# Performance work log

Hardware: AMD Instinct MI355X
Metric: run time of the kernel (lower is better)

## Reference

```python
import jax, jax.numpy as jnp
import numpy as np
from jax import lax

EPS = 1e-6
PPU = 256        # points_per_unit
MULT = 8         # 2 ** rho.num_halving_layers
C = 3            # in_channels (data channels)
NBASIS = 5
NS = 4           # num_samples
RHO_IN = 16      # encoder out / rho in channels
RHO_OUT = 32     # rho out channels
KW = 5           # conv kernel width


def setup_inputs() -> dict:
    key = jax.random.key(0)
    ks = jax.random.split(key, 16)
    nb, npts, ntar = 16, 2048, 256
    x = jax.random.uniform(ks[0], (nb, npts, C), jnp.float32)
    y = jax.random.normal(ks[1], (nb, npts, C), jnp.float32)
    x_out = jax.random.uniform(ks[2], (nb, ntar, C), jnp.float32)
    # --- compute_xgrid (done concretely at setup; mirrors torch logic) ---
    x_min = float(min(np.min(np.asarray(x)), np.min(np.asarray(x_out)))) - 0.1
    x_max = float(max(np.max(np.asarray(x)), np.max(np.asarray(x_out)))) + 0.1
    ngrid = int(np.ceil(PPU * (x_max - x_min) / MULT) * MULT)  # to_multiple
    grid = jnp.linspace(x_min, x_max, ngrid, dtype=jnp.float32)
    x_grid = jnp.broadcast_to(grid[None, :, None], (nb, ngrid, C))
    # --- parameters ---
    init_l = 2.0 / PPU
    enc_sigma = jnp.log(1e-6 + init_l * jnp.ones((C,), jnp.float32))
    int_sigma = jnp.log(1e-6 + init_l * jnp.ones((NBASIS, C), jnp.float32))
    s = 0.05
    gW = s * jax.random.normal(ks[3], (2 * C, RHO_IN), jnp.float32)
    gb = jnp.zeros((RHO_IN,), jnp.float32)
    w1 = s * jax.random.normal(ks[4], (RHO_OUT, RHO_IN, KW), jnp.float32)
    b1 = jnp.zeros((RHO_OUT,), jnp.float32)
    w2 = s * jax.random.normal(ks[5], (RHO_OUT, RHO_OUT, KW), jnp.float32)
    b2 = jnp.zeros((RHO_OUT,), jnp.float32)
    w3 = s * jax.random.normal(ks[6], (RHO_OUT, RHO_OUT, KW), jnp.float32)
    b3 = jnp.zeros((RHO_OUT,), jnp.float32)
    linW = s * jax.random.normal(ks[7], (RHO_OUT, 2 * C * NBASIS), jnp.float32)
    linb = jnp.zeros((2 * C * NBASIS,), jnp.float32)
    loW = s * jax.random.normal(ks[8], (C * NBASIS, 2 * C), jnp.float32)
    lob = jnp.zeros((2 * C,), jnp.float32)
    eps_noise = jax.random.normal(ks[9], (NS, nb, C * NBASIS), jnp.float32)
    return dict(x=x, y=y, x_out=x_out, x_grid=x_grid, eps_noise=eps_noise,
                enc_sigma=enc_sigma, gW=gW, gb=gb, w1=w1, b1=b1, w2=w2, b2=b2,
                w3=w3, b3=b3, linW=linW, linb=linb, int_sigma=int_sigma,
                loW=loW, lob=lob)


def _conv1d(h, w, b):
    # h: (N, Cin, L), w: (Cout, Cin, K) -> (N, Cout, L)
    return lax.conv_general_dilated(h, w, (1,), 'SAME',
                                    dimension_numbers=('NCH', 'OIH', 'NCH')) + b[None, :, None]


def reference(x, y, x_out, x_grid, eps_noise, enc_sigma, gW, gb,
              w1, b1, w2, b2, w3, b3, linW, linb, int_sigma, loW, lob):
    nb = x.shape[0]
    # ---- ConvDeepSet encoder: context points -> grid ----
    scales = jnp.exp(enc_sigma)                                  # (C,)
    d = (x[:, :, None, :] - x_grid[:, None, :, :]) / (scales + EPS)  # (nb,n,m,C)
    wt = jnp.exp(-0.5 * d * d)
    h0 = wt.sum(axis=1)                                          # (nb,m,C)
    h1 = (y[:, :, None, :] * wt).sum(axis=1)                     # (nb,m,C)
    n_h1 = h1 / (h0 + EPS)
    rep = jnp.concatenate([h0, n_h1], axis=-1) @ gW + gb         # (nb,m,RHO_IN)
    # ---- rho CNN on grid ----
    h = jax.nn.sigmoid(rep).transpose(0, 2, 1)                   # (nb,RHO_IN,m)
    h = jax.nn.relu(_conv1d(h, w1, b1))
    h = jax.nn.relu(_conv1d(h, w2, b2))
    h = _conv1d(h, w3, b3)                                       # (nb,RHO_OUT,m)
    h_grid = h.transpose(0, 2, 1) @ linW + linb                  # (nb,m,2*C*NBASIS)
    h_mu, h_std = jnp.split(h_grid, 2, axis=-1)
    h_std = 0.1 + 0.9 * jax.nn.sigmoid(h_std)
    # ---- latent samples ----
    z = h_mu[None] + h_std[None] * eps_noise[:, :, None, :]      # (NS,nb,m,C*NBASIS)
    ngrid = z.shape[2]
    z = z.reshape(NS * nb, ngrid, NBASIS, C)
    # ---- FinalLayer interpolator: grid -> targets ----
    xg = jnp.broadcast_to(x_grid[None], (NS,) + x_grid.shape).reshape(NS * nb, ngrid, C)
    xt = jnp.broadcast_to(x_out[None], (NS,) + x_out.shape).reshape(NS * nb, -1, C)
    iscales = jnp.exp(int_sigma)                                  # (NBASIS,C)
    dd = (xg[:, :, None, None, :] - xt[:, None, :, None, :]) / (iscales + EPS)
    wtt = jnp.exp(-0.5 * dd * dd)                                 # (NSnb,m,t,NBASIS,C)
    h_out = (z[:, :, None, :, :] * wtt).sum(axis=1)               # (NSnb,t,NBASIS,C)
    ntar = h_out.shape[1]
    out = h_out.reshape(NS * nb, ntar, NBASIS * C) @ loW + lob    # (NSnb,t,2C)
    mu, std = jnp.split(out, 2, axis=-1)
    std = jax.nn.softplus(std)
    return jnp.concatenate([mu, std], axis=-1).reshape(NS, nb, ntar, 2 * C)
```

## Files before the change

### kernel.cpp

```cpp
#include <hip/hip_runtime.h>
#include <math.h>

#define EPSF 1e-6f
#define LOG2E 1.4426950408889634f

__device__ __forceinline__ float sigmoidf_(float v) { return 1.0f / (1.0f + __expf(-v)); }

#define W1OFF   0
#define W2OFF   4096
#define W3OFF   0
#define SINOFF  12288
#define SH1OFF  12800
#define SH2OFF  13696
#define SH3TOFF 14464
#define REDOFF  15104
#define TOTOFF  16640
#define RNGOFF  16832

__global__ __launch_bounds__(512, 1) void encrho_kernel(
    const float* __restrict__ x, const float* __restrict__ y,
    const float* __restrict__ xg, const float* __restrict__ enc_sigma,
    const float* __restrict__ gW, const float* __restrict__ gb,
    const float* __restrict__ w1, const float* __restrict__ b1,
    const float* __restrict__ w2, const float* __restrict__ b2,
    const float* __restrict__ w3, const float* __restrict__ b3,
    const float* __restrict__ linW, const float* __restrict__ linb,
    float* __restrict__ mu_t, float* __restrict__ stdv_t,
    int nb, int M)
{
    __shared__ __align__(16) float smem[16840];
    __shared__ int scnt[3];
    float* flt = smem;

    const int tid = threadIdx.x;
    const int lane = tid & 63;
    const int b = blockIdx.y;
    const int c0 = blockIdx.x * 20;
    const int ic = tid & 31, ng = tid >> 5;

    {
        float sg0 = __expf(enc_sigma[0]) + EPSF;
        float sg1 = __expf(enc_sigma[1]) + EPSF;
        float sg2 = __expf(enc_sigma[2]) + EPSF;
        float e20 = -0.5f * LOG2E / (sg0 * sg0);
        float e21 = -0.5f * LOG2E / (sg1 * sg1);
        float e22 = -0.5f * LOG2E / (sg2 * sg2);

        int mg = c0 - 6 + ic;
        bool cv = (mg >= 0 && mg < M);
        float g0 = 0, g1 = 0, g2 = 0;
        if (cv) {
            const float* gp = xg + (size_t)(b * M + mg) * 3;
            g0 = gp[0]; g1 = gp[1]; g2 = gp[2];
        }
        if (tid < 3) scnt[tid] = 0;
        if (tid < 96) {
            int c = tid >> 5;
            int col = c0 - 6 + ic;
            col = col < 0 ? 0 : (col >= M ? M - 1 : col);
            float gv = xg[(size_t)(b * M + col) * 3 + c];
            float gmn = gv, gmx = gv;
            #pragma unroll
            for (int mask = 1; mask <= 16; mask <<= 1) {
                gmn = fminf(gmn, __shfl_xor(gmn, mask, 64));
                gmx = fmaxf(gmx, __shfl_xor(gmx, mask, 64));
            }
            if (ic == 0) {
                float sgc = __expf(enc_sigma[c]) + EPSF;
                smem[RNGOFF + c] = gmn - 10.0f * sgc;
                smem[RNGOFF + 3 + c] = gmx + 10.0f * sgc;
            }
        }
        __syncthreads();
        {
            const float* xb = x + (size_t)b * 6144;
            const float* yb = y + (size_t)b * 6144;
            for (int base = 0; base < 6144; base += 512) {
                int idx = base + tid;
                float xv = xb[idx];
                float yv = yb[idx];
                int c = idx % 3;
                bool pass = (xv >= smem[RNGOFF + c] && xv <= smem[RNGOFF + 3 + c]);
                #pragma unroll
                for (int t = 0; t < 3; t++) {
                    unsigned long long mball = __ballot(pass && (c == t));
                    int bpos = 0;
                    if (lane == 0) bpos = atomicAdd(&scnt[t], __popcll(mball));
                    bpos = __shfl(bpos, 0, 64);
                    if (pass && (c == t)) {
                        int pos = bpos + __popcll(mball & ((1ull << lane) - 1ull));
                        int o = (t << 12) + (pos << 1);
                        flt[o] = xv;
                        flt[o + 1] = yv;
                    }
                }
            }
        }
        __syncthreads();
        if (tid < 96) {
            int c = tid >> 5;
            int cnt = scnt[c];
            int cp = (cnt + 31) & ~31;
            int p = cnt + (tid & 31);
            if (p < cp) {
                int o = (c << 12) + (p << 1);
                flt[o] = 1e30f;
                flt[o + 1] = 0.0f;
            }
        }
        __syncthreads();
        int cp0 = (scnt[0] + 31) & ~31;
        int cp1 = (scnt[1] + 31) & ~31;
        int cp2 = (scnt[2] + 31) & ~31;
        float h[6];
        {
            const float2* f = (const float2*)flt;
            float s0a = 0, s0b = 0, s1a = 0, s1b = 0;
            #pragma unroll 2
            for (int n = ng; n < cp0; n += 32) {
                float2 va = f[n], vb = f[n + 16];
                float da = va.x - g0; float wa = exp2f(e20 * da * da);
                float db = vb.x - g0; float wb = exp2f(e20 * db * db);
                s0a += wa; s1a = fmaf(va.y, wa, s1a);
                s0b += wb; s1b = fmaf(vb.y, wb, s1b);
            }
            h[0] = s0a + s0b; h[3] = s1a + s1b;
        }
        {
            const float2* f = (const float2*)flt + 2048;
            float s0a = 0, s0b = 0, s1a = 0, s1b = 0;
            #pragma unroll 2
            for (int n = ng; n < cp1; n += 32) {
                float2 va = f[n], vb = f[n + 16];
                float da = va.x - g1; float wa = exp2f(e21 * da * da);
                float db = vb.x - g1; float wb = exp2f(e21 * db * db);
                s0a += wa; s1a = fmaf(va.y, wa, s1a);
                s0b += wb; s1b = fmaf(vb.y, wb, s1b);
            }
            h[1] = s0a + s0b; h[4] = s1a + s1b;
        }
        {
            const float2* f = (const float2*)flt + 4096;
            float s0a = 0, s0b = 0, s1a = 0, s1b = 0;
            #pragma unroll 2
            for (int n = ng; n < cp2; n += 32) {
                float2 va = f[n], vb = f[n + 16];
                float da = va.x - g2; float wa = exp2f(e22 * da * da);
                float db = vb.x - g2; float wb = exp2f(e22 * db * db);
                s0a += wa; s1a = fmaf(va.y, wa, s1a);
                s0b += wb; s1b = fmaf(vb.y, wb, s1b);
            }
            h[2] = s0a + s0b; h[5] = s1a + s1b;
        }
        __syncthreads();
        #pragma unroll
        for (int c = 0; c < 6; c++) h[c] += __shfl_xor(h[c], 32, 64);
        int wv = tid >> 6;
        if (lane < 32) {
            float* rp = smem + REDOFF + wv * 192 + lane * 6;
            #pragma unroll
            for (int c = 0; c < 6; c++) rp[c] = h[c];
        }
        {
            const float4* w1v4 = (const float4*)w1;
            const float4* w2v4 = (const float4*)w2;
            #pragma unroll 1
            for (int i4 = tid; i4 < 640; i4 += 512) {
                float4 v = w1v4[i4];
                float vv[4] = {v.x, v.y, v.z, v.w};
                #pragma unroll
                for (int j = 0; j < 4; j++) {
                    int e = 4 * i4 + j;
                    int row = e / 5;
                    smem[W1OFF + row * 8 + (e - row * 5)] = vv[j];
                }
            }
            #pragma unroll 1
            for (int i4 = tid; i4 < 1280; i4 += 512) {
                float4 v = w2v4[i4];
                float vv[4] = {v.x, v.y, v.z, v.w};
                #pragma unroll
                for (int j = 0; j < 4; j++) {
                    int e = 4 * i4 + j;
                    int row = e / 5;
                    smem[W2OFF + row * 8 + (e - row * 5)] = vv[j];
                }
            }
        }
        __syncthreads();
        if (tid < 192) {
            int ic2 = tid & 31, c = tid >> 5;
            float s = 0.0f;
            #pragma unroll
            for (int w = 0; w < 8; w++) s += smem[REDOFF + w * 192 + ic2 * 6 + c];
            smem[TOTOFF + ic2 * 6 + c] = s;
        }
        __syncthreads();
        {
            int j = tid >> 5, ic2 = tid & 31;
            int mg2 = c0 - 6 + ic2;
            float v = 0.0f;
            if (mg2 >= 0 && mg2 < M) {
                const float* tp = smem + TOTOFF + ic2 * 6;
                float cat[6];
                #pragma unroll
                for (int c = 0; c < 3; c++) {
                    cat[c] = tp[c];
                    cat[3 + c] = tp[3 + c] / (tp[c] + EPSF);
                }
                float r = gb[j];
                #pragma unroll
                for (int i = 0; i < 6; i++) r = fmaf(cat[i], gW[i * 16 + j], r);
                v = sigmoidf_(r);
            }
            smem[SINOFF + j * 32 + ic2] = v;
        }
    }
    __syncthreads();

    {
        if (tid < 448) {
            int o = tid / 14, cp = tid - (tid / 14) * 14;
            int q = 2 * cp;
            float a0 = b1[o], a1 = a0;
            #pragma unroll 2
            for (int i = 0; i < 16; i++) {
                const float* ip = smem + SINOFF + i * 32 + q;
                float2 f01 = *(const float2*)ip;
                float2 f23 = *(const float2*)(ip + 2);
                float2 f45 = *(const float2*)(ip + 4);
                const float* wr = smem + W1OFF + (o * 16 + i) * 8;
                float4 wa = *(const float4*)wr; float wa4 = wr[4];
                a0 = fmaf(f01.x, wa.x, a0); a0 = fmaf(f01.y, wa.y, a0);
                a0 = fmaf(f23.x, wa.z, a0); a0 = fmaf(f23.y, wa.w, a0);
                a0 = fmaf(f45.x, wa4, a0);
                a1 = fmaf(f01.y, wa.x, a1); a1 = fmaf(f23.x, wa.y, a1);
                a1 = fmaf(f23.y, wa.z, a1); a1 = fmaf(f45.x, wa.w, a1);
                a1 = fmaf(f45.y, wa4, a1);
            }
            int gq = c0 - 4 + q;
            bool v0 = (gq >= 0 && gq < M), v1 = (gq + 1 >= 0 && gq + 1 < M);
            smem[SH1OFF + o * 28 + q]     = v0 ? fmaxf(a0, 0.f) : 0.f;
            smem[SH1OFF + o * 28 + q + 1] = v1 ? fmaxf(a1, 0.f) : 0.f;
        }
        __syncthreads();
        float4 wreg0, wreg1, wreg2;
        {
            const float4* w3v = (const float4*)w3;
            wreg0 = w3v[tid];
            wreg1 = w3v[tid + 512];
            if (tid < 256) wreg2 = w3v[tid + 1024];
        }
        if (tid < 384) {
            int o = tid / 12, cp = tid - (tid / 12) * 12;
            int q = 2 * cp;
            float a0 = b2[o], a1 = a0;
            #pragma unroll 2
            for (int i = 0; i < 32; i++) {
                const float* ip = smem + SH1OFF + i * 28 + q;
                float2 f01 = *(const float2*)ip;
                float2 f23 = *(const float2*)(ip + 2);
                float2 f45 = *(const float2*)(ip + 4);
                const float* wr = smem + W2OFF + (o * 32 + i) * 8;
                float4 wa = *(const float4*)wr; float wa4 = wr[4];
                a0 = fmaf(f01.x, wa.x, a0); a0 = fmaf(f01.y, wa.y, a0);
                a0 = fmaf(f23.x, wa.z, a0); a0 = fmaf(f23.y, wa.w, a0);
                a0 = fmaf(f45.x, wa4, a0);
                a1 = fmaf(f01.y, wa.x, a1); a1 = fmaf(f23.x, wa.y, a1);
                a1 = fmaf(f23.y, wa.z, a1); a1 = fmaf(f45.x, wa.w, a1);
                a1 = fmaf(f45.y, wa4, a1);
            }
            int gq = c0 - 2 + q;
            bool v0 = (gq >= 0 && gq < M), v1 = (gq + 1 >= 0 && gq + 1 < M);
            smem[SH2OFF + o * 24 + q]     = v0 ? fmaxf(a0, 0.f) : 0.f;
            smem[SH2OFF + o * 24 + q + 1] = v1 ? fmaxf(a1, 0.f) : 0.f;
        }
        __syncthreads();
        {
            float vv0[4] = {wreg0.x, wreg0.y, wreg0.z, wreg0.w};
            #pragma unroll
            for (int j = 0; j < 4; j++) {
                int e = 4 * tid + j;
                int row = e / 5;
                smem[W3OFF + row * 8 + (e - row * 5)] = vv0[j];
            }
            float vv1[4] = {wreg1.x, wreg1.y, wreg1.z, wreg1.w};
            #pragma unroll
            for (int j = 0; j < 4; j++) {
                int e = 4 * (tid + 512) + j;
                int row = e / 5;
                smem[W3OFF + row * 8 + (e - row * 5)] = vv1[j];
            }
            if (tid < 256) {
                float vv2[4] = {wreg2.x, wreg2.y, wreg2.z, wreg2.w};
                #pragma unroll
                for (int j = 0; j < 4; j++) {
                    int e = 4 * (tid + 1024) + j;
                    int row = e / 5;
                    smem[W3OFF + row * 8 + (e - row * 5)] = vv2[j];
                }
            }
        }
        __syncthreads();
        if (tid < 320) {
            int o = tid / 10, cp = tid - (tid / 10) * 10;
            int q = 2 * cp;
            float a0 = b3[o], a1 = a0;
            #pragma unroll 2
            for (int i = 0; i < 32; i++) {
                const float* ip = smem + SH2OFF + i * 24 + q;
                float2 f01 = *(const float2*)ip;
                float2 f23 = *(const float2*)(ip + 2);
                float2 f45 = *(const float2*)(ip + 4);
                const float* wr = smem + W3OFF + (o * 32 + i) * 8;
                float4 wa = *(const float4*)wr; float wa4 = wr[4];
                a0 = fmaf(f01.x, wa.x, a0); a0 = fmaf(f01.y, wa.y, a0);
                a0 = fmaf(f23.x, wa.z, a0); a0 = fmaf(f23.y, wa.w, a0);
                a0 = fmaf(f45.x, wa4, a0);
                a1 = fmaf(f01.y, wa.x, a1); a1 = fmaf(f23.x, wa.y, a1);
                a1 = fmaf(f23.y, wa.z, a1); a1 = fmaf(f45.x, wa.w, a1);
                a1 = fmaf(f45.y, wa4, a1);
            }
            smem[SH3TOFF + q * 32 + o]       = a0;
            smem[SH3TOFF + (q + 1) * 32 + o] = a1;
        }
        __syncthreads();
        #pragma unroll 1
        for (int idx = tid; idx < 600; idx += 512) {
            int q = idx / 30, j = idx - (idx / 30) * 30;
            int m = c0 + q;
            if (m < M) {
                const float* hp = smem + SH3TOFF + q * 32;
                float v = linb[j];
                #pragma unroll
                for (int o4 = 0; o4 < 8; o4++) {
                    float4 h4 = *(const float4*)(hp + o4 * 4);
                    const float* lw = linW + o4 * 4 * 30 + j;
                    v = fmaf(h4.x, lw[0], v);
                    v = fmaf(h4.y, lw[30], v);
                    v = fmaf(h4.z, lw[60], v);
                    v = fmaf(h4.w, lw[90], v);
                }
                if (j < 15) mu_t[((size_t)b * 15 + j) * M + m] = v;
                else        stdv_t[((size_t)b * 15 + (j - 15)) * M + m] = 0.1f + 0.9f * sigmoidf_(v);
            }
        }
    }
}

__global__ __launch_bounds__(256, 4) void final_kernel(
    const float* __restrict__ x_out, const float* __restrict__ xg,
    const float* __restrict__ int_sigma, const float* __restrict__ eps,
    const float* __restrict__ mu_t, const float* __restrict__ stdv_t,
    const float* __restrict__ loW, const float* __restrict__ lob,
    float* __restrict__ out, int nb, int ntar, int M)
{
    __shared__ float AB[8][30];
    int b = blockIdx.y;
    int tt = blockIdx.x * 8;
    int tid = threadIdx.x;
    int mg = tid & 31, ti = tid >> 5;
    int t = tt + ti;
    bool tv = (t < ntar);
    float xt[3];
    #pragma unroll
    for (int c = 0; c < 3; c++) xt[c] = tv ? x_out[((size_t)b * ntar + t) * 3 + c] : 0.0f;
    float k2[15], Wc[3] = {0, 0, 0};
    #pragma unroll
    for (int k = 0; k < 15; k++) {
        float isc = __expf(int_sigma[k]) + EPSF;
        k2[k] = -0.5f * LOG2E / (isc * isc);
        Wc[k % 3] = fmaxf(Wc[k % 3], 10.0f * isc);
    }
    float gg0 = xg[(size_t)b * M * 3];
    float ggL = xg[((size_t)b * M + (M - 1)) * 3];
    float Dx = (ggL - gg0) / (float)(M - 1);
    float invDx = 1.0f / Dx;
    float A[15], B[15];
    #pragma unroll
    for (int k = 0; k < 15; k++) { A[k] = 0.0f; B[k] = 0.0f; }
    #pragma unroll
    for (int c = 0; c < 3; c++) {
        float xtc = xt[c];
        int lo = (int)floorf((xtc - Wc[c] - gg0) * invDx) - 1;
        int hi = (int)ceilf((xtc + Wc[c] - gg0) * invDx) + 1;
        lo = lo < 0 ? 0 : lo;
        hi = hi > M - 1 ? M - 1 : hi;
        const float* pm0 = mu_t + ((size_t)b * 15 + c) * M;
        const float* pm1 = pm0 + 3 * M;
        const float* pm2 = pm0 + 6 * M;
        const float* pm3 = pm0 + 9 * M;
        const float* pm4 = pm0 + 12 * M;
        const float* ps0 = stdv_t + ((size_t)b * 15 + c) * M;
        const float* ps1 = ps0 + 3 * M;
        const float* ps2 = ps0 + 6 * M;
        const float* ps3 = ps0 + 9 * M;
        const float* ps4 = ps0 + 12 * M;
        #pragma unroll 1
        for (int m = lo + mg; m <= hi; m += 32) {
            float d = (gg0 + m * Dx) - xtc;
            float d2 = d * d;
            float w0 = exp2f(k2[c] * d2);
            float w1v = exp2f(k2[c + 3] * d2);
            float w2v = exp2f(k2[c + 6] * d2);
            float w3v = exp2f(k2[c + 9] * d2);
            float w4v = exp2f(k2[c + 12] * d2);
            A[c]      = fmaf(pm0[m], w0, A[c]);       B[c]      = fmaf(ps0[m], w0, B[c]);
            A[c + 3]  = fmaf(pm1[m], w1v, A[c + 3]);  B[c + 3]  = fmaf(ps1[m], w1v, B[c + 3]);
            A[c + 6]  = fmaf(pm2[m], w2v, A[c + 6]);  B[c + 6]  = fmaf(ps2[m], w2v, B[c + 6]);
            A[c + 9]  = fmaf(pm3[m], w3v, A[c + 9]);  B[c + 9]  = fmaf(ps3[m], w3v, B[c + 9]);
            A[c + 12] = fmaf(pm4[m], w4v, A[c + 12]); B[c + 12] = fmaf(ps4[m], w4v, B[c + 12]);
        }
    }
    #pragma unroll
    for (int mask = 1; mask <= 16; mask <<= 1) {
        #pragma unroll
        for (int k = 0; k < 15; k++) {
            A[k] += __shfl_xor(A[k], mask, 64);
            B[k] += __shfl_xor(B[k], mask, 64);
        }
    }
    if (mg == 0) {
        #pragma unroll
        for (int k = 0; k < 15; k++) { AB[ti][k] = A[k]; AB[ti][15 + k] = B[k]; }
    }
    __syncthreads();
    if (tid < 192) {
        int t2 = tid / 24;
        int rem = tid - t2 * 24;
        int s = rem / 6, j = rem - s * 6;
        int tg = tt + t2;
        if (tg < ntar) {
            float val = lob[j];
            const float* ep = eps + ((size_t)s * nb + b) * 15;
            #pragma unroll
            for (int k = 0; k < 15; k++) {
                float h = fmaf(ep[k], AB[t2][15 + k], AB[t2][k]);
                val = fmaf(h, loW[k * 6 + j], val);
            }
            if (j >= 3) val = fmaxf(val, 0.0f) + log1pf(__expf(-fabsf(val)));
            out[(((size_t)s * nb + b) * ntar + tg) * 6 + j] = val;
        }
    }
}


__global__ __launch_bounds__(1024) void enc_kernel_g(
    const float* __restrict__ x, const float* __restrict__ y,
    const float* __restrict__ xg, const float* __restrict__ enc_sigma,
    const float* __restrict__ gW, const float* __restrict__ gb,
    float* __restrict__ rep_s, int nb, int npts, int M)
{
    __shared__ float sx[6144];
    __shared__ float sy[6144];
    __shared__ float red[16][8][6];
    __shared__ float tot[8][6];
    int b = blockIdx.y;
    int mt = blockIdx.x * 8;
    int tid = threadIdx.x;
    int n3 = npts * 3;
    if (n3 > 6144) n3 = 6144;
    for (int i = tid; i < n3; i += 1024) {
        sx[i] = x[(size_t)b * npts * 3 + i];
        sy[i] = y[(size_t)b * npts * 3 + i];
    }
    int npts_l = n3 / 3;
    int mi = tid & 7, ng = tid >> 3;
    int m = mt + mi;
    bool mv = (m < M);
    float e1[3], g[3];
    for (int c = 0; c < 3; c++) {
        float inv = 1.0f / (__expf(enc_sigma[c]) + EPSF);
        e1[c] = -0.5f * inv * inv;
    }
    for (int c = 0; c < 3; c++) g[c] = mv ? xg[(size_t)(b * M + m) * 3 + c] : 0.0f;
    __syncthreads();
    float h0[3] = {0,0,0}, h1[3] = {0,0,0};
    for (int n = ng; n < npts_l; n += 128) {
        for (int c = 0; c < 3; c++) {
            float d = sx[n * 3 + c] - g[c];
            float w = __expf(e1[c] * d * d);
            h0[c] += w;
            h1[c] = fmaf(sy[n * 3 + c], w, h1[c]);
        }
    }
    for (int mask = 8; mask <= 32; mask <<= 1) {
        for (int c = 0; c < 3; c++) {
            h0[c] += __shfl_xor(h0[c], mask, 64);
            h1[c] += __shfl_xor(h1[c], mask, 64);
        }
    }
    int lane = tid & 63, wv = tid >> 6;
    if (lane < 8) {
        for (int c = 0; c < 3; c++) { red[wv][lane][c] = h0[c]; red[wv][lane][3 + c] = h1[c]; }
    }
    __syncthreads();
    if (tid < 48) {
        int mi2 = tid & 7, c2 = tid >> 3;
        float s = 0.0f;
        for (int k = 0; k < 16; k++) s += red[k][mi2][c2];
        tot[mi2][c2] = s;
    }
    __syncthreads();
    if (tid < 128) {
        int mi2 = tid & 7, j = tid >> 3;
        int m2 = mt + mi2;
        if (m2 < M) {
            float cat[6];
            for (int c = 0; c < 3; c++) {
                cat[c] = tot[mi2][c];
                cat[3 + c] = tot[mi2][3 + c] / (tot[mi2][c] + EPSF);
            }
            float r = gb[j];
            for (int i = 0; i < 6; i++) r = fmaf(cat[i], gW[i * 16 + j], r);
            rep_s[((size_t)b * 16 + j) * M + m2] = sigmoidf_(r);
        }
    }
}

__global__ __launch_bounds__(256) void rho_kernel_g(
    const float* __restrict__ rep_s,
    const float* __restrict__ w1, const float* __restrict__ b1,
    const float* __restrict__ w2, const float* __restrict__ b2,
    const float* __restrict__ w3, const float* __restrict__ b3,
    const float* __restrict__ linW, const float* __restrict__ linb,
    float* __restrict__ mu_t, float* __restrict__ stdv_t,
    int nb, int M)
{
    __shared__ float sWA[5152];
    __shared__ float sWB[5152];
    __shared__ float sIn[16][20];
    __shared__ float sH1[32][16];
    __shared__ float sH2[32][12];
    __shared__ float sH3[32][8];
    int b = blockIdx.y;
    int t0 = blockIdx.x * 8;
    int tid = threadIdx.x;
    {
        const float4* w1v = (const float4*)w1;
        const float4* w2v = (const float4*)w2;
        for (int i4 = tid; i4 < 640; i4 += 256) {
            float4 v = w1v[i4];
            float vv[4] = {v.x, v.y, v.z, v.w};
            for (int j = 0; j < 4; j++) {
                int e = 4 * i4 + j;
                sWA[(e / 80) * 81 + e % 80] = vv[j];
            }
        }
        for (int i4 = tid; i4 < 1280; i4 += 256) {
            float4 v = w2v[i4];
            float vv[4] = {v.x, v.y, v.z, v.w};
            for (int j = 0; j < 4; j++) {
                int e = 4 * i4 + j;
                sWB[(e / 160) * 161 + e % 160] = vv[j];
            }
        }
        for (int idx = tid; idx < 16 * 20; idx += 256) {
            int i = idx / 20, q = idx % 20;
            int mg = t0 - 6 + q;
            sIn[i][q] = (mg >= 0 && mg < M) ? rep_s[((size_t)b * 16 + i) * M + mg] : 0.0f;
        }
    }
    __syncthreads();
    int o = tid >> 3, q0 = tid & 7;
    {
        float a0 = b1[o], a1 = a0;
        #pragma unroll 2
        for (int i = 0; i < 16; i++) {
            const float* wp = sWA + o * 81 + i * 5;
            float u0 = wp[0], u1 = wp[1], u2 = wp[2], u3 = wp[3], u4 = wp[4];
            const float* ip = &sIn[i][0];
            a0 = fmaf(ip[q0], u0, a0);      a0 = fmaf(ip[q0+1], u1, a0);
            a0 = fmaf(ip[q0+2], u2, a0);    a0 = fmaf(ip[q0+3], u3, a0);
            a0 = fmaf(ip[q0+4], u4, a0);
            a1 = fmaf(ip[q0+8], u0, a1);    a1 = fmaf(ip[q0+9], u1, a1);
            a1 = fmaf(ip[q0+10], u2, a1);   a1 = fmaf(ip[q0+11], u3, a1);
            a1 = fmaf(ip[q0+12], u4, a1);
        }
        int g0 = t0 - 4 + q0, g1 = g0 + 8;
        sH1[o][q0]     = (g0 >= 0 && g0 < M) ? fmaxf(a0, 0.0f) : 0.0f;
        sH1[o][q0 + 8] = (g1 >= 0 && g1 < M) ? fmaxf(a1, 0.0f) : 0.0f;
    }
    __syncthreads();
    float4 wreg[5];
    {
        const float4* w3v = (const float4*)w3;
        for (int h = 0; h < 5; h++) wreg[h] = w3v[tid + 256 * h];
    }
    {
        float a0 = b2[o], a1 = a0;
        bool second = (q0 < 4);
        #pragma unroll 2
        for (int i = 0; i < 32; i++) {
            const float* wp = sWB + o * 161 + i * 5;
            float u0 = wp[0], u1 = wp[1], u2 = wp[2], u3 = wp[3], u4 = wp[4];
            const float* ip = &sH1[i][0];
            a0 = fmaf(ip[q0], u0, a0);      a0 = fmaf(ip[q0+1], u1, a0);
            a0 = fmaf(ip[q0+2], u2, a0);    a0 = fmaf(ip[q0+3], u3, a0);
            a0 = fmaf(ip[q0+4], u4, a0);
            if (second) {
                a1 = fmaf(ip[q0+8], u0, a1);    a1 = fmaf(ip[q0+9], u1, a1);
                a1 = fmaf(ip[q0+10], u2, a1);   a1 = fmaf(ip[q0+11], u3, a1);
                a1 = fmaf(ip[q0+12], u4, a1);
            }
        }
        int g0 = t0 - 2 + q0, g1 = g0 + 8;
        sH2[o][q0] = (g0 >= 0 && g0 < M) ? fmaxf(a0, 0.0f) : 0.0f;
        if (second) sH2[o][q0 + 8] = (g1 >= 0 && g1 < M) ? fmaxf(a1, 0.0f) : 0.0f;
    }
    __syncthreads();
    for (int h = 0; h < 5; h++) {
        float vv[4] = {wreg[h].x, wreg[h].y, wreg[h].z, wreg[h].w};
        for (int j = 0; j < 4; j++) {
            int e = 4 * (tid + 256 * h) + j;
            sWA[(e / 160) * 161 + e % 160] = vv[j];
        }
    }
    __syncthreads();
    {
        float a0 = b3[o];
        #pragma unroll 2
        for (int i = 0; i < 32; i++) {
            const float* wp = sWA + o * 161 + i * 5;
            float u0 = wp[0], u1 = wp[1], u2 = wp[2], u3 = wp[3], u4 = wp[4];
            const float* ip = &sH2[i][0];
            a0 = fmaf(ip[q0], u0, a0);      a0 = fmaf(ip[q0+1], u1, a0);
            a0 = fmaf(ip[q0+2], u2, a0);    a0 = fmaf(ip[q0+3], u3, a0);
            a0 = fmaf(ip[q0+4], u4, a0);
        }
        sH3[o][q0] = a0;
    }
    __syncthreads();
    if (tid < 240) {
        int q = tid / 30, j = tid % 30;
        int m = t0 + q;
        if (m < M) {
            float v = linb[j];
            #pragma unroll 8
            for (int oo = 0; oo < 32; oo++) v = fmaf(sH3[oo][q], linW[oo * 30 + j], v);
            if (j < 15) mu_t[((size_t)b * 15 + j) * M + m] = v;
            else        stdv_t[((size_t)b * 15 + (j - 15)) * M + m] = 0.1f + 0.9f * sigmoidf_(v);
        }
    }
}

extern "C" void kernel_launch(void* const* d_in, const int* in_sizes, int n_in,
                              void* d_out, int out_size, void* d_ws, size_t ws_size,
                              hipStream_t stream)
{
    const float* x         = (const float*)d_in[0];
    const float* y         = (const float*)d_in[1];
    const float* x_out     = (const float*)d_in[2];
    const float* x_grid    = (const float*)d_in[3];
    const float* eps_noise = (const float*)d_in[4];
    const float* enc_sigma = (const float*)d_in[5];
    const float* gW        = (const float*)d_in[6];
    const float* gb        = (const float*)d_in[7];
    const float* w1        = (const float*)d_in[8];
    const float* b1        = (const float*)d_in[9];
    const float* w2        = (const float*)d_in[10];
    const float* b2        = (const float*)d_in[11];
    const float* w3        = (const float*)d_in[12];
    const float* b3        = (const float*)d_in[13];
    const float* linW      = (const float*)d_in[14];
    const float* linb      = (const float*)d_in[15];
    const float* int_sigma = (const float*)d_in[16];
    const float* loW       = (const float*)d_in[17];
    const float* lob       = (const float*)d_in[18];
    float* out = (float*)d_out;

    const int NS = 4, C = 3, NBASIS = 5;
    int nb   = in_sizes[4] / (NS * C * NBASIS);
    int npts = in_sizes[0] / (nb * C);
    int ntar = in_sizes[2] / (nb * C);
    int M    = in_sizes[3] / (nb * C);

    float* mu_t   = (float*)d_ws;
    float* stdv_t = mu_t + (size_t)nb * 15 * M;

    bool fast = (npts == 2048 && M <= 320);
    if (fast) {
        encrho_kernel<<<dim3(16, nb), 512, 0, stream>>>(
            x, y, x_grid, enc_sigma, gW, gb,
            w1, b1, w2, b2, w3, b3, linW, linb, mu_t, stdv_t, nb, M);
    } else {
        float* rep_s = stdv_t + (size_t)nb * 15 * M;
        enc_kernel_g<<<dim3((M + 7) / 8, nb), 1024, 0, stream>>>(
            x, y, x_grid, enc_sigma, gW, gb, rep_s, nb, npts, M);
        rho_kernel_g<<<dim3((M + 7) / 8, nb), 256, 0, stream>>>(
            rep_s, w1, b1, w2, b2, w3, b3, linW, linb, mu_t, stdv_t, nb, M);
    }
    final_kernel<<<dim3((ntar + 7) / 8, nb), 256, 0, stream>>>(
        x_out, x_grid, int_sigma, eps_noise, mu_t, stdv_t, loW, lob, out, nb, ntar, M);
}
```

Measured before the change: 42.49 us.

## Halve encoder-rho tile width to double block count and remap conv threads

Each encrho block now produces 10 grid columns instead of 20, with the grid sized from M. That doubles the number of blocks to fill more CUs, but each block recomputes a larger relative halo and repeats the x/y filtering pass. The three conv layers are remapped to one output channel per 16 threads with one or two columns each, replacing the paired float2 scheme. The point-filtering ballot/popcount compaction is replaced by per-element shared atomics, which is simpler but may contend more.

```diff
diff --git a/kernel.cpp b/kernel.cpp
--- a/kernel.cpp
+++ b/kernel.cpp
@@ -10,12 +10,12 @@
 #define W2OFF   4096
 #define W3OFF   0
 #define SINOFF  12288
-#define SH1OFF  12800
-#define SH2OFF  13696
-#define SH3TOFF 14464
-#define REDOFF  15104
-#define TOTOFF  16640
-#define RNGOFF  16832
+#define SH1OFF  12640
+#define SH2OFF  13216
+#define SH3TOFF 13664
+#define REDOFF  13984
+#define TOTOFF  15520
+#define RNGOFF  15712
 
 __global__ __launch_bounds__(512, 1) void encrho_kernel(
     const float* __restrict__ x, const float* __restrict__ y,
@@ -28,14 +28,13 @@
     float* __restrict__ mu_t, float* __restrict__ stdv_t,
     int nb, int M)
 {
-    __shared__ __align__(16) float smem[16840];
+    __shared__ __align__(16) float smem[15718];
     __shared__ int scnt[3];
     float* flt = smem;
 
     const int tid = threadIdx.x;
-    const int lane = tid & 63;
     const int b = blockIdx.y;
-    const int c0 = blockIdx.x * 20;
+    const int c0 = blockIdx.x * 10;
     const int ic = tid & 31, ng = tid >> 5;
 
     {
@@ -47,7 +46,7 @@
         float e22 = -0.5f * LOG2E / (sg2 * sg2);
 
         int mg = c0 - 6 + ic;
-        bool cv = (mg >= 0 && mg < M);
+        bool cv = (ic < 22) && (mg >= 0) && (mg < M);
         float g0 = 0, g1 = 0, g2 = 0;
         if (cv) {
             const float* gp = xg + (size_t)(b * M + mg) * 3;
@@ -56,7 +55,8 @@
         if (tid < 3) scnt[tid] = 0;
         if (tid < 96) {
             int c = tid >> 5;
-            int col = c0 - 6 + ic;
+            int icc = ic < 22 ? ic : 21;
+            int col = c0 - 6 + icc;
             col = col < 0 ? 0 : (col >= M ? M - 1 : col);
             float gv = xg[(size_t)(b * M + col) * 3 + c];
             float gmn = gv, gmx = gv;
@@ -75,24 +75,15 @@
         {
             const float* xb = x + (size_t)b * 6144;
             const float* yb = y + (size_t)b * 6144;
-            for (int base = 0; base < 6144; base += 512) {
-                int idx = base + tid;
+            #pragma unroll 1
+            for (int idx = tid; idx < 6144; idx += 512) {
                 float xv = xb[idx];
-                float yv = yb[idx];
                 int c = idx % 3;
-                bool pass = (xv >= smem[RNGOFF + c] && xv <= smem[RNGOFF + 3 + c]);
-                #pragma unroll
-                for (int t = 0; t < 3; t++) {
-                    unsigned long long mball = __ballot(pass && (c == t));
-                    int bpos = 0;
-                    if (lane == 0) bpos = atomicAdd(&scnt[t], __popcll(mball));
-                    bpos = __shfl(bpos, 0, 64);
-                    if (pass && (c == t)) {
-                        int pos = bpos + __popcll(mball & ((1ull << lane) - 1ull));
-                        int o = (t << 12) + (pos << 1);
-                        flt[o] = xv;
-                        flt[o + 1] = yv;
-                    }
+                if (xv >= smem[RNGOFF + c] && xv <= smem[RNGOFF + 3 + c]) {
+                    int p = atomicAdd(&scnt[c], 1);
+                    int o = (c << 12) + (p << 1);
+                    flt[o] = xv;
+                    flt[o + 1] = yb[idx];
                 }
             }
         }
@@ -155,7 +146,7 @@
         __syncthreads();
         #pragma unroll
         for (int c = 0; c < 6; c++) h[c] += __shfl_xor(h[c], 32, 64);
-        int wv = tid >> 6;
+        int lane = tid & 63, wv = tid >> 6;
         if (lane < 32) {
             float* rp = smem + REDOFF + wv * 192 + lane * 6;
             #pragma unroll
@@ -198,50 +189,50 @@
         __syncthreads();
         {
             int j = tid >> 5, ic2 = tid & 31;
-            int mg2 = c0 - 6 + ic2;
-            float v = 0.0f;
-            if (mg2 >= 0 && mg2 < M) {
-                const float* tp = smem + TOTOFF + ic2 * 6;
-                float cat[6];
-                #pragma unroll
-                for (int c = 0; c < 3; c++) {
-                    cat[c] = tp[c];
-                    cat[3 + c] = tp[3 + c] / (tp[c] + EPSF);
+            if (ic2 < 22) {
+                int mg2 = c0 - 6 + ic2;
+                float v = 0.0f;
+                if (mg2 >= 0 && mg2 < M) {
+                    const float* tp = smem + TOTOFF + ic2 * 6;
+                    float cat[6];
+                    #pragma unroll
+                    for (int c = 0; c < 3; c++) {
+                        cat[c] = tp[c];
+                        cat[3 + c] = tp[3 + c] / (tp[c] + EPSF);
+                    }
+                    float r = gb[j];
+                    #pragma unroll
+                    for (int i = 0; i < 6; i++) r = fmaf(cat[i], gW[i * 16 + j], r);
+                    v = sigmoidf_(r);
                 }
-                float r = gb[j];
-                #pragma unroll
-                for (int i = 0; i < 6; i++) r = fmaf(cat[i], gW[i * 16 + j], r);
-                v = sigmoidf_(r);
-            }
-            smem[SINOFF + j * 32 + ic2] = v;
+                smem[SINOFF + j * 22 + ic2] = v;
+            }
         }
     }
     __syncthreads();
 
     {
-        if (tid < 448) {
-            int o = tid / 14, cp = tid - (tid / 14) * 14;
-            int q = 2 * cp;
+        int o = tid >> 4, q0 = tid & 15;
+        {
             float a0 = b1[o], a1 = a0;
+            bool two = (q0 < 2);
             #pragma unroll 2
             for (int i = 0; i < 16; i++) {
-                const float* ip = smem + SINOFF + i * 32 + q;
-                float2 f01 = *(const float2*)ip;
-                float2 f23 = *(const float2*)(ip + 2);
-                float2 f45 = *(const float2*)(ip + 4);
-                const float* wr = smem + W1OFF + (o * 16 + i) * 8;
-                float4 wa = *(const float4*)wr; float wa4 = wr[4];
-                a0 = fmaf(f01.x, wa.x, a0); a0 = fmaf(f01.y, wa.y, a0);
-                a0 = fmaf(f23.x, wa.z, a0); a0 = fmaf(f23.y, wa.w, a0);
-                a0 = fmaf(f45.x, wa4, a0);
-                a1 = fmaf(f01.y, wa.x, a1); a1 = fmaf(f23.x, wa.y, a1);
-                a1 = fmaf(f23.y, wa.z, a1); a1 = fmaf(f45.x, wa.w, a1);
-                a1 = fmaf(f45.y, wa4, a1);
-            }
-            int gq = c0 - 4 + q;
-            bool v0 = (gq >= 0 && gq < M), v1 = (gq + 1 >= 0 && gq + 1 < M);
-            smem[SH1OFF + o * 28 + q]     = v0 ? fmaxf(a0, 0.f) : 0.f;
-            smem[SH1OFF + o * 28 + q + 1] = v1 ? fmaxf(a1, 0.f) : 0.f;
+                const float* wp = smem + W1OFF + (o * 16 + i) * 8;
+                float u0 = wp[0], u1 = wp[1], u2 = wp[2], u3 = wp[3], u4 = wp[4];
+                const float* ip = smem + SINOFF + i * 22;
+                a0 = fmaf(ip[q0], u0, a0);     a0 = fmaf(ip[q0+1], u1, a0);
+                a0 = fmaf(ip[q0+2], u2, a0);   a0 = fmaf(ip[q0+3], u3, a0);
+                a0 = fmaf(ip[q0+4], u4, a0);
+                if (two) {
+                    a1 = fmaf(ip[q0+16], u0, a1);  a1 = fmaf(ip[q0+17], u1, a1);
+                    a1 = fmaf(ip[q0+18], u2, a1);  a1 = fmaf(ip[q0+19], u3, a1);
+                    a1 = fmaf(ip[q0+20], u4, a1);
+                }
+            }
+            int g0c = c0 - 4 + q0, g1c = g0c + 16;
+            smem[SH1OFF + o * 18 + q0] = (g0c >= 0 && g0c < M) ? fmaxf(a0, 0.f) : 0.f;
+            if (two) smem[SH1OFF + o * 18 + q0 + 16] = (g1c >= 0 && g1c < M) ? fmaxf(a1, 0.f) : 0.f;
         }
         __syncthreads();
         float4 wreg0, wreg1, wreg2;
@@ -251,29 +242,19 @@
             wreg1 = w3v[tid + 512];
             if (tid < 256) wreg2 = w3v[tid + 1024];
         }
-        if (tid < 384) {
-            int o = tid / 12, cp = tid - (tid / 12) * 12;
-            int q = 2 * cp;
-            float a0 = b2[o], a1 = a0;
+        if (q0 < 14) {
+            float a0 = b2[o];
             #pragma unroll 2
             for (int i = 0; i < 32; i++) {
-                const float* ip = smem + SH1OFF + i * 28 + q;
-                float2 f01 = *(const float2*)ip;
-                float2 f23 = *(const float2*)(ip + 2);
-                float2 f45 = *(const float2*)(ip + 4);
-                const float* wr = smem + W2OFF + (o * 32 + i) * 8;
-                float4 wa = *(const float4*)wr; float wa4 = wr[4];
-                a0 = fmaf(f01.x, wa.x, a0); a0 = fmaf(f01.y, wa.y, a0);
-                a0 = fmaf(f23.x, wa.z, a0); a0 = fmaf(f23.y, wa.w, a0);
-                a0 = fmaf(f45.x, wa4, a0);
-                a1 = fmaf(f01.y, wa.x, a1); a1 = fmaf(f23.x, wa.y, a1);
-                a1 = fmaf(f23.y, wa.z, a1); a1 = fmaf(f45.x, wa.w, a1);
-                a1 = fmaf(f45.y, wa4, a1);
-            }
-            int gq = c0 - 2 + q;
-            bool v0 = (gq >= 0 && gq < M), v1 = (gq + 1 >= 0 && gq + 1 < M);
-            smem[SH2OFF + o * 24 + q]     = v0 ? fmaxf(a0, 0.f) : 0.f;
-            smem[SH2OFF + o * 24 + q + 1] = v1 ? fmaxf(a1, 0.f) : 0.f;
+                const float* wp = smem + W2OFF + (o * 32 + i) * 8;
+                float u0 = wp[0], u1 = wp[1], u2 = wp[2], u3 = wp[3], u4 = wp[4];
+                const float* ip = smem + SH1OFF + i * 18;
+                a0 = fmaf(ip[q0], u0, a0);     a0 = fmaf(ip[q0+1], u1, a0);
+                a0 = fmaf(ip[q0+2], u2, a0);   a0 = fmaf(ip[q0+3], u3, a0);
+                a0 = fmaf(ip[q0+4], u4, a0);
+            }
+            int g0c = c0 - 2 + q0;
+            smem[SH2OFF + o * 14 + q0] = (g0c >= 0 && g0c < M) ? fmaxf(a0, 0.f) : 0.f;
         }
         __syncthreads();
         {
@@ -302,32 +283,22 @@
             }
         }
         __syncthreads();
-        if (tid < 320) {
-            int o = tid / 10, cp = tid - (tid / 10) * 10;
-            int q = 2 * cp;
-            float a0 = b3[o], a1 = a0;
+        if (q0 < 10) {
+            float a0 = b3[o];
             #pragma unroll 2
             for (int i = 0; i < 32; i++) {
-                const float* ip = smem + SH2OFF + i * 24 + q;
-                float2 f01 = *(const float2*)ip;
-                float2 f23 = *(const float2*)(ip + 2);
-                float2 f45 = *(const float2*)(ip + 4);
-                const float* wr = smem + W3OFF + (o * 32 + i) * 8;
-                float4 wa = *(const float4*)wr; float wa4 = wr[4];
-                a0 = fmaf(f01.x, wa.x, a0); a0 = fmaf(f01.y, wa.y, a0);
-                a0 = fmaf(f23.x, wa.z, a0); a0 = fmaf(f23.y, wa.w, a0);
-                a0 = fmaf(f45.x, wa4, a0);
-                a1 = fmaf(f01.y, wa.x, a1); a1 = fmaf(f23.x, wa.y, a1);
-                a1 = fmaf(f23.y, wa.z, a1); a1 = fmaf(f45.x, wa.w, a1);
-                a1 = fmaf(f45.y, wa4, a1);
-            }
-            smem[SH3TOFF + q * 32 + o]       = a0;
-            smem[SH3TOFF + (q + 1) * 32 + o] = a1;
-        }
-        __syncthreads();
-        #pragma unroll 1
-        for (int idx = tid; idx < 600; idx += 512) {
-            int q = idx / 30, j = idx - (idx / 30) * 30;
+                const float* wp = smem + W3OFF + (o * 32 + i) * 8;
+                float u0 = wp[0], u1 = wp[1], u2 = wp[2], u3 = wp[3], u4 = wp[4];
+                const float* ip = smem + SH2OFF + i * 14;
+                a0 = fmaf(ip[q0], u0, a0);     a0 = fmaf(ip[q0+1], u1, a0);
+                a0 = fmaf(ip[q0+2], u2, a0);   a0 = fmaf(ip[q0+3], u3, a0);
+                a0 = fmaf(ip[q0+4], u4, a0);
+            }
+            smem[SH3TOFF + q0 * 32 + o] = a0;
+        }
+        __syncthreads();
+        if (tid < 300) {
+            int q = tid / 30, j = tid - (tid / 30) * 30;
             int m = c0 + q;
             if (m < M) {
                 const float* hp = smem + SH3TOFF + q * 32;
@@ -680,7 +651,8 @@
 
     bool fast = (npts == 2048 && M <= 320);
     if (fast) {
-        encrho_kernel<<<dim3(16, nb), 512, 0, stream>>>(
+        int tiles = (M + 9) / 10;
+        encrho_kernel<<<dim3(tiles, nb), 512, 0, stream>>>(
             x, y, x_grid, enc_sigma, gW, gb,
             w1, b1, w2, b2, w3, b3, linW, linb, mu_t, stdv_t, nb, M);
     } else {
```

Measured after the change: 45.19 us. +6.4%, slower.
